# Performance work log

Hardware: AMD Instinct MI355X
Metric: run time of the kernel (lower is better)

Reference implementation:

```python
import jax, jax.numpy as jnp
import numpy as np

B, T, C, H = 2048, 81, 128, 4
HD = C // H  # head dim = 32


def sudoku_mask():
    # att[i,j] = 0 if cells i,j share a row, column, or 3x3 block; else -inf.
    idx = np.arange(81)
    row, col = idx // 9, idx % 9
    block_a, block_b = col // 3, row // 3  # equality test matches original's swapped naming
    same = (row[:, None] == row[None, :]) | (col[:, None] == col[None, :]) | (
        (block_a[:, None] == block_a[None, :]) & (block_b[:, None] == block_b[None, :]))
    return jnp.asarray(np.where(same, 0.0, -np.inf), dtype=jnp.float32)


def setup_inputs() -> dict:
    key = jax.random.key(0)
    ks = jax.random.split(key, 7)
    s = 1.0 / np.sqrt(C)
    return {
        "x": jax.random.normal(ks[0], (B, T, C), jnp.float32),
        "key_value_states": jax.random.normal(ks[1], (B, T, C), jnp.float32),
        "Wq": jax.random.normal(ks[2], (C, C), jnp.float32) * s,
        "bq": jnp.zeros((C,), jnp.float32),
        "Wk": jax.random.normal(ks[3], (C, C), jnp.float32) * s,
        "bk": jnp.zeros((C,), jnp.float32),
        "Wv": jax.random.normal(ks[4], (C, C), jnp.float32) * s,
        "bv": jnp.zeros((C,), jnp.float32),
        "Wp": jax.random.normal(ks[5], (C, C), jnp.float32) * s,
        "bp": jnp.zeros((C,), jnp.float32),
    }


def reference(x, key_value_states, Wq, bq, Wk, bk, Wv, bv, Wp, bp):
    mask = sudoku_mask()  # [T, Te]
    # projections -> [B, H, T, HD]
    q = (x @ Wq + bq).reshape(B, T, H, HD).transpose(0, 2, 1, 3)
    k = (key_value_states @ Wk + bk).reshape(B, T, H, HD).transpose(0, 2, 1, 3)
    v = (key_value_states @ Wv + bv).reshape(B, T, H, HD).transpose(0, 2, 1, 3)
    att = jnp.einsum("bhqd,bhkd->bhqk", q, k) * (1.0 / np.sqrt(HD))
    att = att + mask  # broadcast over [B, H]
    att_to_check = att  # pre-softmax scores (the clone in torch)
    p = jax.nn.softmax(att, axis=-1)  # attn_drop is identity (p=0 / eval)
    y = jnp.einsum("bhqk,bhkd->bhqd", p, v)
    y = y.transpose(0, 2, 1, 3).reshape(B, T, C)
    y = y @ Wp + bp  # resid_drop is identity
    return (y, att_to_check)
```

## Files before the change

kernel.cpp:

```cpp
#include <hip/hip_runtime.h>
#include <math.h>

namespace {
constexpr int NB = 2048;
constexpr int TT = 81;
constexpr int CC = 128;
constexpr int NH = 4;
constexpr int HD = 32;
constexpr int BT  = TT * CC;
constexpr int ATTS = NH * TT * TT;
constexpr int MT = NB * TT / 64;
constexpr float SCALE = 0.17677669529663687f;
constexpr float MASKED = -1.0e30f;
}

__device__ __forceinline__ int swz(int row, int k) {
    return row * CC + (k ^ ((row & 7) << 2));
}

struct MaskTab { unsigned w[TT][4]; };
constexpr MaskTab make_mask() {
    MaskTab t{};
    for (int i = 0; i < TT; ++i) {
        const int ri = i / 9, ci = i % 9;
        for (int j = 0; j < TT; ++j) {
            const int rj = j / 9, cj = j % 9;
            const bool same = (ri == rj) || (ci == cj) ||
                              ((ri / 3 == rj / 3) && (ci / 3 == cj / 3));
            if (same) t.w[i][j >> 5] |= 1u << (j & 31);
        }
    }
    return t;
}
__device__ __constant__ MaskTab MASKT = make_mask();

__global__ __launch_bounds__(512, 4)
void qkv_gemm(const float* __restrict__ x, const float* __restrict__ kvs,
              const float* __restrict__ Wq, const float* __restrict__ bq,
              const float* __restrict__ Wk, const float* __restrict__ bk,
              const float* __restrict__ Wv, const float* __restrict__ bv,
              float* __restrict__ qk_region,
              float* __restrict__ v_region,
              size_t qk_stride)
{
    __shared__ float act[2 * 64 * CC];

    const int tid = threadIdx.x;
    const size_t gbase = (size_t)blockIdx.x * 64 * CC;

    for (int t = tid; t < 64 * CC / 4; t += 512) {
        const int row = t >> 5;
        const int k0  = (t & 31) << 2;
        const int d   = swz(row, k0);
        *reinterpret_cast<float4*>(&act[d]) =
            *reinterpret_cast<const float4*>(x + gbase + t * 4);
        *reinterpret_cast<float4*>(&act[64 * CC + d]) =
            *reinterpret_cast<const float4*>(kvs + gbase + t * 4);
    }
    __syncthreads();

    const int lane = tid & 63;
    const int wid  = __builtin_amdgcn_readfirstlane(tid >> 6);
    const int m    = blockIdx.x * 64 + lane;
    const int bb   = m / TT;
    const int ii   = m - bb * TT;

    for (int cg = 0; cg < 3; ++cg) {
        const int G    = cg * 8 + wid;
        const int sel  = G >> 3;
        const int col0 = (G & 7) << 4;
        const float* W    = (sel == 0) ? Wq : (sel == 1) ? Wk : Wv;
        const float* bias = (sel == 0) ? bq : (sel == 1) ? bk : bv;
        const int abase   = (sel == 0) ? 0 : 64 * CC;

        float acc[16];
        #pragma unroll
        for (int c = 0; c < 16; ++c) acc[c] = bias[col0 + c];

        for (int k4 = 0; k4 < 32; ++k4) {
            const float4 a =
                *reinterpret_cast<const float4*>(&act[abase + swz(lane, k4 * 4)]);
            const float* wr = W + (k4 * 4) * CC + col0;
            #pragma unroll
            for (int kk = 0; kk < 4; ++kk) {
                const float av = (kk == 0) ? a.x : (kk == 1) ? a.y
                               : (kk == 2) ? a.z : a.w;
                #pragma unroll
                for (int c4 = 0; c4 < 4; ++c4) {
                    const float4 w =
                        *reinterpret_cast<const float4*>(wr + kk * CC + c4 * 4);
                    acc[c4 * 4 + 0] = fmaf(av, w.x, acc[c4 * 4 + 0]);
                    acc[c4 * 4 + 1] = fmaf(av, w.y, acc[c4 * 4 + 1]);
                    acc[c4 * 4 + 2] = fmaf(av, w.z, acc[c4 * 4 + 2]);
                    acc[c4 * 4 + 3] = fmaf(av, w.w, acc[c4 * 4 + 3]);
                }
            }
        }

        float* dst = (sel == 2)
            ? v_region  + (size_t)bb * BT + ii * CC + col0
            : qk_region + (size_t)bb * qk_stride + (size_t)sel * BT + ii * CC + col0;
        #pragma unroll
        for (int c4 = 0; c4 < 4; ++c4)
            reinterpret_cast<float4*>(dst)[c4] =
                make_float4(acc[c4*4+0], acc[c4*4+1], acc[c4*4+2], acc[c4*4+3]);
    }
}

__global__ __launch_bounds__(256, 3)
void attn_head(const float* __restrict__ qk_ws,
               float* __restrict__ att_region,
               float* __restrict__ yv_region)
{
    __shared__ float Qh[TT * HD];
    __shared__ float Vh[TT * HD];
    __shared__ float Su[TT * TT];

    const int bh  = blockIdx.x;
    const int b   = bh >> 2;
    const int h   = bh & 3;
    const int tid = threadIdx.x;

    const float* qbase = qk_ws + (size_t)b * 2 * BT;
    const float* kbase = qbase + BT;
    float* vbase = yv_region + (size_t)b * BT;
    float* abase = att_region + (size_t)b * ATTS + (size_t)h * TT * TT;

    for (int t = tid; t < TT * 8; t += 256) {
        const int i  = t >> 3;
        const int c4 = (t & 7) << 2;
        const float4 qv = *reinterpret_cast<const float4*>(qbase + i * CC + h * HD + c4);
        const float4 vv = *reinterpret_cast<const float4*>(vbase + i * CC + h * HD + c4);
        const float4 kv = *reinterpret_cast<const float4*>(kbase + i * CC + h * HD + c4);
        *reinterpret_cast<float4*>(&Qh[i * HD + c4]) = qv;
        *reinterpret_cast<float4*>(&Vh[i * HD + c4]) = vv;
        Su[i * 33 + c4 + 0] = kv.x;
        Su[i * 33 + c4 + 1] = kv.y;
        Su[i * 33 + c4 + 2] = kv.z;
        Su[i * 33 + c4 + 3] = kv.w;
    }
    __syncthreads();

    const int io = tid / 41;
    const int jg = tid - io * 41;
    const bool sact = tid < 246;
    const int j0 = jg * 2;
    const int j1 = j0 + 1;
    const bool hasj1 = j1 < TT;
    const int j1r = hasj1 ? j1 : j0;

    float k0[HD], k1[HD];
    if (sact) {
        #pragma unroll
        for (int c = 0; c < HD; ++c) {
            k0[c] = Su[j0 * 33 + c];
            k1[c] = Su[j1r * 33 + c];
        }
    }
    __syncthreads();

    if (sact) {
        const int w0 = j0 >> 5, s0b = j0 & 31;
        const int w1 = j1 >> 5, s1b = j1 & 31;
        const int i0   = (io < 3) ? io * 14 : 42 + (io - 3) * 13;
        const int ilen = (io < 3) ? 14 : 13;
        for (int t = 0; t < ilen; ++t) {
            const int i = i0 + t;
            const float4* qf = reinterpret_cast<const float4*>(&Qh[i * HD]);
            float s0 = 0.f, s1 = 0.f;
            #pragma unroll
            for (int c4 = 0; c4 < 8; ++c4) {
                const float4 q4 = qf[c4];
                s0 = fmaf(q4.x, k0[c4*4+0], s0); s0 = fmaf(q4.y, k0[c4*4+1], s0);
                s0 = fmaf(q4.z, k0[c4*4+2], s0); s0 = fmaf(q4.w, k0[c4*4+3], s0);
                s1 = fmaf(q4.x, k1[c4*4+0], s1); s1 = fmaf(q4.y, k1[c4*4+1], s1);
                s1 = fmaf(q4.z, k1[c4*4+2], s1); s1 = fmaf(q4.w, k1[c4*4+3], s1);
            }
            const unsigned mw0 = MASKT.w[i][w0];
            Su[i * TT + j0] = ((mw0 >> s0b) & 1u) ? s0 * SCALE : MASKED;
            if (hasj1) {
                const unsigned mw1 = MASKT.w[i][w1];
                Su[i * TT + j1] = ((mw1 >> s1b) & 1u) ? s1 * SCALE : MASKED;
            }
        }
    }
    __syncthreads();

    for (int e = tid; e < TT * TT; e += 256)
        abase[e] = Su[e];

    if (tid < 2 * TT) {
        const int ph = tid / TT;
        const int pi = tid - ph * TT;
        const int d0 = ph * 16;
        const float* srow = &Su[pi * TT];

        float m0 = -INFINITY, m1 = -INFINITY, m2 = -INFINITY;
        for (int j = 0; j < TT; j += 3) {
            m0 = fmaxf(m0, srow[j + 0]);
            m1 = fmaxf(m1, srow[j + 1]);
            m2 = fmaxf(m2, srow[j + 2]);
        }
        const float mx = fmaxf(m0, fmaxf(m1, m2));

        float acc[16];
        #pragma unroll
        for (int c = 0; c < 16; ++c) acc[c] = 0.f;
        float sum = 0.f;
        for (int j = 0; j < TT; ++j) {
            const float e = __expf(srow[j] - mx);
            sum += e;
            const float4* vr = reinterpret_cast<const float4*>(&Vh[j * HD + d0]);
            #pragma unroll
            for (int c4 = 0; c4 < 4; ++c4) {
                const float4 v4 = vr[c4];
                acc[c4 * 4 + 0] = fmaf(e, v4.x, acc[c4 * 4 + 0]);
                acc[c4 * 4 + 1] = fmaf(e, v4.y, acc[c4 * 4 + 1]);
                acc[c4 * 4 + 2] = fmaf(e, v4.z, acc[c4 * 4 + 2]);
                acc[c4 * 4 + 3] = fmaf(e, v4.w, acc[c4 * 4 + 3]);
            }
        }
        const float inv = 1.0f / sum;
        float* dst = vbase + pi * CC + h * HD + d0;
        #pragma unroll
        for (int c4 = 0; c4 < 4; ++c4)
            reinterpret_cast<float4*>(dst)[c4] =
                make_float4(acc[c4*4+0]*inv, acc[c4*4+1]*inv,
                            acc[c4*4+2]*inv, acc[c4*4+3]*inv);
    }
}

__global__ __launch_bounds__(1024, 4)
void attn_fused(float* __restrict__ att_region, float* __restrict__ yv_region)
{
    __shared__ float Kl[TT * CC];
    __shared__ float Vl[TT * CC];
    __shared__ float scmp[NH * TT * 21];
    __shared__ signed char slotT[TT * TT];

    const int b   = blockIdx.x;
    const int tid = threadIdx.x;
    float* abase = att_region + (size_t)b * ATTS;
    float* vbase = yv_region  + (size_t)b * BT;

    if (tid < TT) {
        const int i = tid, ri = i / 9, ci = i - ri * 9;
        int cnt = 0;
        for (int j = 0; j < TT; ++j) {
            const int rj = j / 9, cj = j - rj * 9;
            const bool same = (ri == rj) | (ci == cj) |
                              ((ri / 3 == rj / 3) & (ci / 3 == cj / 3));
            slotT[i * TT + j] = same ? (signed char)(cnt++) : (signed char)(-1);
        }
    }
    for (int t = tid; t < BT / 4; t += 1024) {
        reinterpret_cast<float4*>(Kl)[t] =
            reinterpret_cast<const float4*>(abase + BT)[t];
        reinterpret_cast<float4*>(Vl)[t] =
            reinterpret_cast<const float4*>(vbase)[t];
    }
    __syncthreads();

    const int p = tid;
    int h = 0, half = 0, i = 0;
    if (p < 2 * NH * TT) {
        h = p / (2 * TT);
        const int rem = p - h * 2 * TT;
        half = rem / TT;
        i = rem - half * TT;
    }

    if (p < 2 * NH * TT) {
        float q[HD];
        const float* qr = abase + i * CC + h * HD;
        #pragma unroll
        for (int c4 = 0; c4 < 8; ++c4) {
            const float4 t4 = *reinterpret_cast<const float4*>(qr + c4 * 4);
            q[c4*4+0] = t4.x; q[c4*4+1] = t4.y; q[c4*4+2] = t4.z; q[c4*4+3] = t4.w;
        }
        const signed char* srow = &slotT[i * TT];
        const int rbase = (h * TT + i) * 21;
        const int j0 = half ? 41 : 0;
        const int j1 = half ? TT : 41;
        for (int j = j0; j < j1; ++j) {
            const float* kr = &Kl[j * CC + h * HD];
            float p0 = 0.f, p1 = 0.f, p2 = 0.f, p3 = 0.f;
            #pragma unroll
            for (int c4 = 0; c4 < 8; c4 += 4) {
                const float4 k0 = *reinterpret_cast<const float4*>(kr + (c4+0)*4);
                const float4 k1 = *reinterpret_cast<const float4*>(kr + (c4+1)*4);
                const float4 k2 = *reinterpret_cast<const float4*>(kr + (c4+2)*4);
                const float4 k3 = *reinterpret_cast<const float4*>(kr + (c4+3)*4);
                p0 = fmaf(q[c4*4+ 0], k0.x, p0); p0 = fmaf(q[c4*4+ 1], k0.y, p0);
                p0 = fmaf(q[c4*4+ 2], k0.z, p0); p0 = fmaf(q[c4*4+ 3], k0.w, p0);
                p1 = fmaf(q[c4*4+ 4], k1.x, p1); p1 = fmaf(q[c4*4+ 5], k1.y, p1);
                p1 = fmaf(q[c4*4+ 6], k1.z, p1); p1 = fmaf(q[c4*4+ 7], k1.w, p1);
                p2 = fmaf(q[c4*4+ 8], k2.x, p2); p2 = fmaf(q[c4*4+ 9], k2.y, p2);
                p2 = fmaf(q[c4*4+10], k2.z, p2); p2 = fmaf(q[c4*4+11], k2.w, p2);
                p3 = fmaf(q[c4*4+12], k3.x, p3); p3 = fmaf(q[c4*4+13], k3.y, p3);
                p3 = fmaf(q[c4*4+14], k3.z, p3); p3 = fmaf(q[c4*4+15], k3.w, p3);
            }
            const float s = ((p0 + p1) + (p2 + p3)) * SCALE;
            const int sl = srow[j];
            if (sl >= 0) scmp[rbase + sl] = s;
        }
    }
    __syncthreads();

    for (int e4 = tid; e4 < ATTS / 4; e4 += 1024) {
        float4 o;
        float* op = reinterpret_cast<float*>(&o);
        #pragma unroll
        for (int u = 0; u < 4; ++u) {
            const int e   = e4 * 4 + u;
            const int row = e / TT;
            const int j   = e - row * TT;
            const int i2  = row - (row / TT) * TT;
            const int sl  = slotT[i2 * TT + j];
            op[u] = (sl >= 0) ? scmp[row * 21 + sl] : MASKED;
        }
        reinterpret_cast<float4*>(abase)[e4] = o;
    }

    if (p < 2 * NH * TT) {
        const int rbase = (h * TT + i) * 21;
        const int dim0  = h * HD + half * 16;
        float mx = -INFINITY;
        #pragma unroll
        for (int s = 0; s < 21; ++s) mx = fmaxf(mx, scmp[rbase + s]);

        float acc[16];
        #pragma unroll
        for (int c = 0; c < 16; ++c) acc[c] = 0.f;
        float sum = 0.f;
        const signed char* srow = &slotT[i * TT];
        for (int j = 0; j < TT; ++j) {
            const int sl  = srow[j];
            const int sli = sl < 0 ? 0 : sl;
            const float sv = scmp[rbase + sli];
            const float e  = (sl >= 0) ? __expf(sv - mx) : 0.0f;
            sum += e;
            const float* vr = &Vl[j * CC + dim0];
            #pragma unroll
            for (int c4 = 0; c4 < 4; ++c4) {
                const float4 v4 = *reinterpret_cast<const float4*>(vr + c4 * 4);
                acc[c4*4+0] = fmaf(e, v4.x, acc[c4*4+0]);
                acc[c4*4+1] = fmaf(e, v4.y, acc[c4*4+1]);
                acc[c4*4+2] = fmaf(e, v4.z, acc[c4*4+2]);
                acc[c4*4+3] = fmaf(e, v4.w, acc[c4*4+3]);
            }
        }
        const float inv = 1.0f / sum;
        float* dst = vbase + i * CC + dim0;
        #pragma unroll
        for (int c4 = 0; c4 < 4; ++c4)
            reinterpret_cast<float4*>(dst)[c4] =
                make_float4(acc[c4*4+0]*inv, acc[c4*4+1]*inv,
                            acc[c4*4+2]*inv, acc[c4*4+3]*inv);
    }
}

__global__ __launch_bounds__(512, 8)
void out_gemm(float* __restrict__ y_region,
              const float* __restrict__ Wp, const float* __restrict__ bp)
{
    __shared__ float yl[64 * CC];

    const int tid = threadIdx.x;
    const size_t gbase = (size_t)blockIdx.x * 64 * CC;

    for (int t = tid; t < 64 * CC / 4; t += 512) {
        const int row = t >> 5;
        const int k0  = (t & 31) << 2;
        *reinterpret_cast<float4*>(&yl[swz(row, k0)]) =
            *reinterpret_cast<const float4*>(y_region + gbase + t * 4);
    }
    __syncthreads();

    const int lane = tid & 63;
    const int wid  = __builtin_amdgcn_readfirstlane(tid >> 6);
    const int col0 = wid << 4;

    float acc[16];
    #pragma unroll
    for (int c = 0; c < 16; ++c) acc[c] = bp[col0 + c];

    for (int k4 = 0; k4 < 32; ++k4) {
        const float4 a = *reinterpret_cast<const float4*>(&yl[swz(lane, k4 * 4)]);
        const float* wr = Wp + (k4 * 4) * CC + col0;
        #pragma unroll
        for (int kk = 0; kk < 4; ++kk) {
            const float av = (kk == 0) ? a.x : (kk == 1) ? a.y
                           : (kk == 2) ? a.z : a.w;
            #pragma unroll
            for (int c4 = 0; c4 < 4; ++c4) {
                const float4 w =
                    *reinterpret_cast<const float4*>(wr + kk * CC + c4 * 4);
                acc[c4*4+0] = fmaf(av, w.x, acc[c4*4+0]);
                acc[c4*4+1] = fmaf(av, w.y, acc[c4*4+1]);
                acc[c4*4+2] = fmaf(av, w.z, acc[c4*4+2]);
                acc[c4*4+3] = fmaf(av, w.w, acc[c4*4+3]);
            }
        }
    }

    float* dst = y_region + gbase + lane * CC + col0;
    #pragma unroll
    for (int c4 = 0; c4 < 4; ++c4)
        reinterpret_cast<float4*>(dst)[c4] =
            make_float4(acc[c4*4+0], acc[c4*4+1], acc[c4*4+2], acc[c4*4+3]);
}

extern "C" void kernel_launch(void* const* d_in, const int* in_sizes, int n_in,
                              void* d_out, int out_size, void* d_ws, size_t ws_size,
                              hipStream_t stream) {
    (void)in_sizes; (void)n_in; (void)out_size;
    const float* x   = (const float*)d_in[0];
    const float* kvs = (const float*)d_in[1];
    const float* Wq  = (const float*)d_in[2];
    const float* bq  = (const float*)d_in[3];
    const float* Wk  = (const float*)d_in[4];
    const float* bk  = (const float*)d_in[5];
    const float* Wv  = (const float*)d_in[6];
    const float* bv  = (const float*)d_in[7];
    const float* Wp  = (const float*)d_in[8];
    const float* bp  = (const float*)d_in[9];

    float* ybase   = (float*)d_out;
    float* attbase = ybase + (size_t)NB * BT;

    const size_t need = (size_t)NB * 2 * BT * sizeof(float);
    if (ws_size >= need) {
        float* qkws = (float*)d_ws;
        qkv_gemm<<<MT, 512, 0, stream>>>(x, kvs, Wq, bq, Wk, bk, Wv, bv,
                                         qkws, ybase, (size_t)(2 * BT));
        attn_head<<<NB * NH, 256, 0, stream>>>(qkws, attbase, ybase);
    } else {
        qkv_gemm<<<MT, 512, 0, stream>>>(x, kvs, Wq, bq, Wk, bk, Wv, bv,
                                         attbase, ybase, (size_t)ATTS);
        attn_fused<<<NB, 1024, 0, stream>>>(attbase, ybase);
    }
    out_gemm<<<MT, 512, 0, stream>>>(ybase, Wp, bp);
}
```

Measured before the change: 555.4 us.

## Split QKV GEMM across grid y per projection and force vector weight loads

The QKV projection kernel now launches one block per projection along grid y, so each block stages only one activation tile in shared memory, halving LDS use. The key/value input tile is read twice from global memory as a result. An opaque zero offset on the weight pointer makes weight reads per-lane vector loads rather than scalar loads, and the k-loop is partially unrolled. out_gemm gets the same load change, a lower occupancy bound, and a barrier before its in-place store.

New measurement: 1.490 ms. 168% more time.

```diff
diff --git a/kernel.cpp b/kernel.cpp
--- a/kernel.cpp
+++ b/kernel.cpp
@@ -18,6 +18,12 @@
     return row * CC + (k ^ ((row & 7) << 2));
 }
 
+__device__ __forceinline__ int opaque_zero() {
+    int vz;
+    asm volatile("v_mov_b32 %0, 0" : "=v"(vz));
+    return vz;
+}
+
 struct MaskTab { unsigned w[TT][4]; };
 constexpr MaskTab make_mask() {
     MaskTab t{};
@@ -43,68 +49,61 @@
               float* __restrict__ v_region,
               size_t qk_stride)
 {
-    __shared__ float act[2 * 64 * CC];
+    __shared__ float act[64 * CC];
 
     const int tid = threadIdx.x;
+    const int sel = blockIdx.y;
+    const float* W    = (sel == 0) ? Wq : (sel == 1) ? Wk : Wv;
+    const float* bias = (sel == 0) ? bq : (sel == 1) ? bk : bv;
+    const float* src  = (sel == 0) ? x  : kvs;
     const size_t gbase = (size_t)blockIdx.x * 64 * CC;
 
     for (int t = tid; t < 64 * CC / 4; t += 512) {
         const int row = t >> 5;
         const int k0  = (t & 31) << 2;
-        const int d   = swz(row, k0);
-        *reinterpret_cast<float4*>(&act[d]) =
-            *reinterpret_cast<const float4*>(x + gbase + t * 4);
-        *reinterpret_cast<float4*>(&act[64 * CC + d]) =
-            *reinterpret_cast<const float4*>(kvs + gbase + t * 4);
+        *reinterpret_cast<float4*>(&act[swz(row, k0)]) =
+            *reinterpret_cast<const float4*>(src + gbase + t * 4);
     }
     __syncthreads();
 
     const int lane = tid & 63;
-    const int wid  = __builtin_amdgcn_readfirstlane(tid >> 6);
+    const int col0 = (tid >> 6) << 4;
+    const int vz   = opaque_zero();
     const int m    = blockIdx.x * 64 + lane;
     const int bb   = m / TT;
     const int ii   = m - bb * TT;
 
-    for (int cg = 0; cg < 3; ++cg) {
-        const int G    = cg * 8 + wid;
-        const int sel  = G >> 3;
-        const int col0 = (G & 7) << 4;
-        const float* W    = (sel == 0) ? Wq : (sel == 1) ? Wk : Wv;
-        const float* bias = (sel == 0) ? bq : (sel == 1) ? bk : bv;
-        const int abase   = (sel == 0) ? 0 : 64 * CC;
-
-        float acc[16];
-        #pragma unroll
-        for (int c = 0; c < 16; ++c) acc[c] = bias[col0 + c];
-
-        for (int k4 = 0; k4 < 32; ++k4) {
-            const float4 a =
-                *reinterpret_cast<const float4*>(&act[abase + swz(lane, k4 * 4)]);
-            const float* wr = W + (k4 * 4) * CC + col0;
-            #pragma unroll
-            for (int kk = 0; kk < 4; ++kk) {
-                const float av = (kk == 0) ? a.x : (kk == 1) ? a.y
-                               : (kk == 2) ? a.z : a.w;
-                #pragma unroll
-                for (int c4 = 0; c4 < 4; ++c4) {
-                    const float4 w =
-                        *reinterpret_cast<const float4*>(wr + kk * CC + c4 * 4);
-                    acc[c4 * 4 + 0] = fmaf(av, w.x, acc[c4 * 4 + 0]);
-                    acc[c4 * 4 + 1] = fmaf(av, w.y, acc[c4 * 4 + 1]);
-                    acc[c4 * 4 + 2] = fmaf(av, w.z, acc[c4 * 4 + 2]);
-                    acc[c4 * 4 + 3] = fmaf(av, w.w, acc[c4 * 4 + 3]);
-                }
-            }
-        }
-
-        float* dst = (sel == 2)
-            ? v_region  + (size_t)bb * BT + ii * CC + col0
-            : qk_region + (size_t)bb * qk_stride + (size_t)sel * BT + ii * CC + col0;
-        #pragma unroll
-        for (int c4 = 0; c4 < 4; ++c4)
-            reinterpret_cast<float4*>(dst)[c4] =
-                make_float4(acc[c4*4+0], acc[c4*4+1], acc[c4*4+2], acc[c4*4+3]);
-    }
+    float acc[16];
+    #pragma unroll
+    for (int c = 0; c < 16; ++c) acc[c] = bias[col0 + c];
+
+    #pragma unroll 4
+    for (int k4 = 0; k4 < 32; ++k4) {
+        const float4 a = *reinterpret_cast<const float4*>(&act[swz(lane, k4 * 4)]);
+        const float* wr = W + (size_t)(k4 * 4) * CC + col0 + vz;
+        #pragma unroll
+        for (int kk = 0; kk < 4; ++kk) {
+            const float av = (kk == 0) ? a.x : (kk == 1) ? a.y
+                           : (kk == 2) ? a.z : a.w;
+            #pragma unroll
+            for (int c4 = 0; c4 < 4; ++c4) {
+                const float4 w =
+                    *reinterpret_cast<const float4*>(wr + kk * CC + c4 * 4);
+                acc[c4 * 4 + 0] = fmaf(av, w.x, acc[c4 * 4 + 0]);
+                acc[c4 * 4 + 1] = fmaf(av, w.y, acc[c4 * 4 + 1]);
+                acc[c4 * 4 + 2] = fmaf(av, w.z, acc[c4 * 4 + 2]);
+                acc[c4 * 4 + 3] = fmaf(av, w.w, acc[c4 * 4 + 3]);
+            }
+        }
+    }
+
+    float* dst = (sel == 2)
+        ? v_region  + (size_t)bb * BT + ii * CC + col0
+        : qk_region + (size_t)bb * qk_stride + (size_t)sel * BT + ii * CC + col0;
+    #pragma unroll
+    for (int c4 = 0; c4 < 4; ++c4)
+        reinterpret_cast<float4*>(dst)[c4] =
+            make_float4(acc[c4*4+0], acc[c4*4+1], acc[c4*4+2], acc[c4*4+3]);
 }
 
 __global__ __launch_bounds__(256, 3)
@@ -360,7 +359,7 @@
     }
 }
 
-__global__ __launch_bounds__(512, 8)
+__global__ __launch_bounds__(512, 6)
 void out_gemm(float* __restrict__ y_region,
               const float* __restrict__ Wp, const float* __restrict__ bp)
 {
@@ -378,16 +377,17 @@
     __syncthreads();
 
     const int lane = tid & 63;
-    const int wid  = __builtin_amdgcn_readfirstlane(tid >> 6);
-    const int col0 = wid << 4;
+    const int col0 = (tid >> 6) << 4;
+    const int vz   = opaque_zero();
 
     float acc[16];
     #pragma unroll
     for (int c = 0; c < 16; ++c) acc[c] = bp[col0 + c];
 
+    #pragma unroll 4
     for (int k4 = 0; k4 < 32; ++k4) {
         const float4 a = *reinterpret_cast<const float4*>(&yl[swz(lane, k4 * 4)]);
-        const float* wr = Wp + (k4 * 4) * CC + col0;
+        const float* wr = Wp + (size_t)(k4 * 4) * CC + col0 + vz;
         #pragma unroll
         for (int kk = 0; kk < 4; ++kk) {
             const float av = (kk == 0) ? a.x : (kk == 1) ? a.y
@@ -403,6 +403,8 @@
             }
         }
     }
+
+    __syncthreads();
 
     float* dst = y_region + gbase + lane * CC + col0;
     #pragma unroll
@@ -432,12 +434,12 @@
     const size_t need = (size_t)NB * 2 * BT * sizeof(float);
     if (ws_size >= need) {
         float* qkws = (float*)d_ws;
-        qkv_gemm<<<MT, 512, 0, stream>>>(x, kvs, Wq, bq, Wk, bk, Wv, bv,
-                                         qkws, ybase, (size_t)(2 * BT));
+        qkv_gemm<<<dim3(MT, 3), 512, 0, stream>>>(x, kvs, Wq, bq, Wk, bk, Wv, bv,
+                                                  qkws, ybase, (size_t)(2 * BT));
         attn_head<<<NB * NH, 256, 0, stream>>>(qkws, attbase, ybase);
     } else {
-        qkv_gemm<<<MT, 512, 0, stream>>>(x, kvs, Wq, bq, Wk, bk, Wv, bv,
-                                         attbase, ybase, (size_t)ATTS);
+        qkv_gemm<<<dim3(MT, 3), 512, 0, stream>>>(x, kvs, Wq, bq, Wk, bk, Wv, bv,
+                                                  attbase, ybase, (size_t)ATTS);
         attn_fused<<<NB, 1024, 0, stream>>>(attbase, ybase);
     }
     out_gemm<<<MT, 512, 0, stream>>>(ybase, Wp, bp);
```
